# Kernel optimization log

Hardware: AMD Instinct MI355X
Metric: run time of the kernel (lower is better)

The kernel has to match this reference:

```python
import jax, jax.numpy as jnp
import numpy as np

SCALE = 10.0
TEMP = 0.5
SIM_TH = 0.7
EPOCH = 1
KL_WEIGHT = max(0.5 * (1 - EPOCH / 60), 0.1)
NEG_INF = -1e30


def _normalize(x, eps=1e-12):
    n = jnp.linalg.norm(x, axis=-1, keepdims=True)
    return x / jnp.maximum(n, eps)


def setup_inputs() -> dict:
    key = jax.random.key(0)
    ks = jax.random.split(key, 6)
    P, B, D, N, K = 4, 128, 512, 32768, 10
    # 0.02 scale keeps pairwise distances O(1) so exp(-SCALE*dist) does not underflow
    feature = jax.random.normal(ks[0], (P, B, D), jnp.float32) * 0.02
    text_feature = jax.random.normal(ks[1], (B, P, D), jnp.float32) * 0.02
    centers = jax.random.normal(ks[2], (P, N, D), jnp.float32) * 0.02
    position = jax.random.randint(ks[3], (B,), 0, N)
    cross_indices = jax.random.randint(ks[4], (B, K), 0, N)
    vid = jax.random.randint(ks[5], (N,), 0, 751)
    return {"feature": feature, "text_feature": text_feature, "centers": centers,
            "position": position, "cross_indices": cross_indices, "vid": vid}


def _align_loss(feature, text_feature):
    # feature: [P,B,D]; text_feature: [B,P,D] (detached in original)
    img = _normalize(feature)
    txt = _normalize(jax.lax.stop_gradient(jnp.transpose(text_feature, (1, 0, 2))))
    img_sim = jnp.einsum('pbd,pcd->pbc', img, img) / TEMP   # [P,B,B]
    txt_sim = jnp.einsum('pbd,pcd->pbc', txt, txt) / TEMP
    mask = (img_sim > SIM_TH) & (txt_sim > SIM_TH)
    valid = mask.any(-1)                                   # [P,B] row/col validity
    colm = valid[:, None, :]                               # mask over columns
    il = jnp.where(colm, img_sim, NEG_INF)
    tl = jnp.where(colm, txt_sim, NEG_INF)
    img_logp = jax.nn.log_softmax(il, -1)
    txt_logp = jax.nn.log_softmax(tl, -1)                  # fully detached (txt detached)
    txt_prob = jnp.exp(txt_logp)
    img_logp_sg = jax.lax.stop_gradient(img_logp)
    img_prob = jnp.exp(img_logp_sg)
    # F.kl_div(input=log q, target=p) = sum p*(log p - log q), batchmean over valid rows
    kl1 = jnp.sum(jnp.where(colm, txt_prob * (txt_logp - img_logp), 0.0), -1)      # [P,B]
    kl2 = jnp.sum(jnp.where(colm, img_prob * (img_logp_sg - txt_logp), 0.0), -1)
    nvalid = valid.sum(-1)                                 # [P]
    r1 = jnp.sum(jnp.where(valid, kl1, 0.0), -1)
    r2 = jnp.sum(jnp.where(valid, kl2, 0.0), -1)
    per_part = 0.5 * (r1 + r2) / jnp.maximum(nvalid, 1)
    return jnp.sum(jnp.where(nvalid > 0, per_part, 0.0))


def _contrastive_loss(feature, centers, position, cross_indices):
    P, B, D = feature.shape
    N = centers.shape[1]
    pos_feats = jnp.take(centers, cross_indices, axis=1)   # [P,B,K,D]
    fn2 = jnp.sum(feature * feature, -1)                   # [P,B]
    pn2 = jnp.sum(pos_feats * pos_feats, -1)               # [P,B,K]
    pd2 = fn2[..., None] + pn2 - 2.0 * jnp.einsum('pbd,pbkd->pbk', feature, pos_feats)
    pos_dist = jnp.sqrt(jnp.maximum(pd2, 1e-12))           # [P,B,K]
    cn2 = jnp.sum(centers * centers, -1)                   # [P,N]
    nd2 = fn2[..., None] + cn2[:, None, :] - 2.0 * jnp.einsum('pbd,pnd->pbn', feature, centers)
    neg_dist = jnp.sqrt(jnp.maximum(nd2, 1e-12))           # [P,B,N]
    neg_mask = (jnp.ones((N,), bool)
                .at[cross_indices.reshape(-1)].set(False)
                .at[position].set(False))
    x = jnp.log(jnp.sum(jnp.exp(-SCALE * pos_dist), -1))   # [P,B]
    ey = jnp.exp(-SCALE * neg_dist) * neg_mask[None, None, :].astype(neg_dist.dtype)
    y = jnp.log(jnp.sum(ey, -1))                           # [P,B]
    l = jnp.sum(y - x, -1) / B                             # per-part, div by feature.size(1)
    l = jnp.where(jnp.isnan(l), 0.0, l)
    return jnp.sum(l) / P


def reference(feature, text_feature, centers, position, cross_indices, vid):
    align_loss = _align_loss(feature, text_feature)
    contrastive_loss = _contrastive_loss(feature, centers, position, cross_indices)
    total_loss = contrastive_loss + KL_WEIGHT * align_loss
    pos_vid = jnp.take(vid, cross_indices, axis=0)         # [B,K]
    return total_loss, contrastive_loss, align_loss, pos_vid
```

## Files before the change

kernel.cpp:

```cpp
#include <hip/hip_runtime.h>
#include <hip/hip_bf16.h>
#include <math.h>

#define P_ 4
#define B_ 128
#define D_ 512
#define N_ 32768
#define K_ 10
#define TNB 128
#define NT2 (N_ / TNB)
#define BKC 64
#define KP 72

typedef __attribute__((ext_vector_type(8))) short bf16x8;
typedef __attribute__((ext_vector_type(4))) float f32x4;

static __device__ __forceinline__ float block_sum_128(float v, float* sh) {
    const int t = threadIdx.x;
    sh[t] = v; __syncthreads();
    #pragma unroll
    for (int s = 64; s > 0; s >>= 1) { if (t < s) sh[t] += sh[t + s]; __syncthreads(); }
    float r = sh[0]; __syncthreads();
    return r;
}

static __device__ __forceinline__ uint2 pack_bf16x4(float4 v) {
    union { __hip_bfloat162 h; unsigned u; } lo, hi;
    lo.h = __float22bfloat162_rn(make_float2(v.x, v.y));
    hi.h = __float22bfloat162_rn(make_float2(v.z, v.w));
    uint2 r; r.x = lo.u; r.y = hi.u;
    return r;
}

__global__ void prep_kernel(const float* __restrict__ feature,
                            unsigned short* __restrict__ featbf,
                            float* __restrict__ maskf) {
    int i = blockIdx.x * 256 + threadIdx.x;
    float4 v = ((const float4*)feature)[i];
    ((uint2*)featbf)[i] = pack_bf16x4(v);
    if (i < N_) maskf[i] = 1.0f;
}

__global__ void mask_zero_kernel(const int* __restrict__ cross,
                                 const int* __restrict__ pos,
                                 float* __restrict__ m) {
    int i = blockIdx.x * 256 + threadIdx.x;
    if (i < B_ * K_) m[cross[i]] = 0.0f;
    else if (i < B_ * K_ + B_) m[pos[i - B_ * K_]] = 0.0f;
}

__global__ void norm_kernel(const float* __restrict__ feature,
                            const float* __restrict__ text_feature,
                            float* __restrict__ img, float* __restrict__ txt,
                            float* __restrict__ fn2) {
    const int pb = blockIdx.x;
    const int p = pb >> 7, b = pb & 127;
    const int which = blockIdx.y;
    const int t = threadIdx.x;
    const float* src = (which == 0) ? feature + (size_t)pb * D_
                                    : text_feature + ((size_t)b * P_ + p) * D_;
    float v0 = src[t], v1 = src[t + 256];
    __shared__ float sred[256];
    sred[t] = v0 * v0 + v1 * v1;
    __syncthreads();
    #pragma unroll
    for (int s = 128; s > 0; s >>= 1) { if (t < s) sred[t] += sred[t + s]; __syncthreads(); }
    const float ss = sred[0];
    const float inv = 1.0f / fmaxf(sqrtf(ss), 1e-12f);
    float* dst = (which == 0) ? img : txt;
    dst[(size_t)pb * D_ + t] = v0 * inv;
    dst[(size_t)pb * D_ + t + 256] = v1 * inv;
    if (which == 0 && t == 0) fn2[pb] = ss;
}

__global__ void sim_kernel(const float* __restrict__ img,
                           const float* __restrict__ txt,
                           float* __restrict__ img_sim,
                           float* __restrict__ txt_sim,
                           float* __restrict__ validf) {
    const int p = blockIdx.x;
    const int b0 = blockIdx.y * 2;
    const int c = threadIdx.x;
    __shared__ float ai[2][D_];
    __shared__ float at[2][D_];
    __shared__ int flags[2];
    #pragma unroll
    for (int i = 0; i < 8; ++i) {
        int idx = c + i * 128;
        int row = idx >> 9, d = idx & 511;
        ai[row][d] = img[(size_t)(p * B_ + b0 + row) * D_ + d];
        at[row][d] = txt[(size_t)(p * B_ + b0 + row) * D_ + d];
    }
    if (c < 2) flags[c] = 0;
    __syncthreads();
    float di[2] = {0, 0};
    float dt[2] = {0, 0};
    const float* ic = img + (size_t)(p * B_ + c) * D_;
    const float* tc = txt + (size_t)(p * B_ + c) * D_;
    for (int d = 0; d < D_; d += 4) {
        float4 vi = *(const float4*)(ic + d);
        float4 vt = *(const float4*)(tc + d);
        #pragma unroll
        for (int i = 0; i < 2; ++i) {
            di[i] += ai[i][d] * vi.x + ai[i][d + 1] * vi.y + ai[i][d + 2] * vi.z + ai[i][d + 3] * vi.w;
            dt[i] += at[i][d] * vt.x + at[i][d + 1] * vt.y + at[i][d + 2] * vt.z + at[i][d + 3] * vt.w;
        }
    }
    #pragma unroll
    for (int i = 0; i < 2; ++i) {
        float is = 2.0f * di[i];
        float ts = 2.0f * dt[i];
        img_sim[(size_t)(p * B_ + b0 + i) * B_ + c] = is;
        txt_sim[(size_t)(p * B_ + b0 + i) * B_ + c] = ts;
        if (is > 0.7f && ts > 0.7f) flags[i] = 1;
    }
    __syncthreads();
    if (c < 2) validf[p * B_ + b0 + c] = (float)flags[c];
}

__global__ __launch_bounds__(256) void kl_kernel(
    const float* __restrict__ img_sim,
    const float* __restrict__ txt_sim,
    const float* __restrict__ validf,
    float* __restrict__ klrow) {
    const int l = threadIdx.x & 63;
    const int wv = threadIdx.x >> 6;
    const int p = blockIdx.x;
    const int r = blockIdx.y * 4 + wv;
    const size_t base = (size_t)(p * B_ + r) * B_;
    const bool v0 = validf[p * B_ + l] > 0.5f;
    const bool v1 = validf[p * B_ + 64 + l] > 0.5f;
    const float il0 = v0 ? img_sim[base + l] : -1e30f;
    const float il1 = v1 ? img_sim[base + 64 + l] : -1e30f;
    const float tl0 = v0 ? txt_sim[base + l] : -1e30f;
    const float tl1 = v1 ? txt_sim[base + 64 + l] : -1e30f;
    float mi = fmaxf(il0, il1), mt = fmaxf(tl0, tl1);
    #pragma unroll
    for (int off = 32; off > 0; off >>= 1) {
        mi = fmaxf(mi, __shfl_xor(mi, off));
        mt = fmaxf(mt, __shfl_xor(mt, off));
    }
    float si = expf(il0 - mi) + expf(il1 - mi);
    float st = expf(tl0 - mt) + expf(tl1 - mt);
    #pragma unroll
    for (int off = 32; off > 0; off >>= 1) {
        si += __shfl_xor(si, off);
        st += __shfl_xor(st, off);
    }
    const float lsei = mi + logf(si);
    const float lset = mt + logf(st);
    float term = 0.0f;
    if (v0) {
        float lpi = il0 - lsei, lpt = tl0 - lset;
        term += expf(lpt) * (lpt - lpi) + expf(lpi) * (lpi - lpt);
    }
    if (v1) {
        float lpi = il1 - lsei, lpt = tl1 - lset;
        term += expf(lpt) * (lpt - lpi) + expf(lpi) * (lpi - lpt);
    }
    #pragma unroll
    for (int off = 32; off > 0; off >>= 1) term += __shfl_xor(term, off);
    if (l == 0) klrow[p * B_ + r] = (validf[p * B_ + r] > 0.5f) ? term : 0.0f;
}

__global__ void posx_kernel(const float* __restrict__ feature,
                            const float* __restrict__ centers,
                            const float* __restrict__ fn2,
                            const int* __restrict__ cross,
                            float* __restrict__ xarr) {
    const int pb = blockIdx.x;
    const int p = pb >> 7, b = pb & 127;
    const int l = threadIdx.x;
    const float* f = feature + (size_t)pb * D_;
    float4 f0 = *(const float4*)(f + l * 4);
    float4 f1 = *(const float4*)(f + 256 + l * 4);
    const float fn2v = fn2[pb];
    float ex = 0.0f;
    #pragma unroll
    for (int k = 0; k < K_; ++k) {
        int idx = cross[b * K_ + k];
        const float* cp = centers + ((size_t)p * N_ + idx) * D_;
        float4 c0 = *(const float4*)(cp + l * 4);
        float4 c1 = *(const float4*)(cp + 256 + l * 4);
        float dot = f0.x * c0.x + f0.y * c0.y + f0.z * c0.z + f0.w * c0.w
                  + f1.x * c1.x + f1.y * c1.y + f1.z * c1.z + f1.w * c1.w;
        float pn2 = c0.x * c0.x + c0.y * c0.y + c0.z * c0.z + c0.w * c0.w
                  + c1.x * c1.x + c1.y * c1.y + c1.z * c1.z + c1.w * c1.w;
        #pragma unroll
        for (int off = 32; off > 0; off >>= 1) {
            dot += __shfl_down(dot, off);
            pn2 += __shfl_down(pn2, off);
        }
        if (l == 0) {
            float d2 = fn2v + pn2 - 2.0f * dot;
            ex += expf(-10.0f * sqrtf(fmaxf(d2, 1e-12f)));
        }
    }
    if (l == 0) xarr[pb] = logf(ex);
}

__global__ __launch_bounds__(256) void neg_mfma_kernel(
    const unsigned short* __restrict__ featbf,
    const float* __restrict__ centers,
    const float* __restrict__ fn2,
    const float* __restrict__ maskf,
    float* __restrict__ Spart) {
    const int tile = blockIdx.x;
    const int p = blockIdx.y;
    const int n0g = tile * TNB;
    const int t = threadIdx.x;
    const int l = t & 63;
    const int w = t >> 6;
    const int m0w = (w & 1) * 64;
    const int n0w = (w >> 1) * 64;

    __shared__ unsigned short Bs[2][128 * KP];
    __shared__ float cn2s[128];
    __shared__ float red[128];
    __shared__ float fn2s[128];

    if (t < 128) { red[t] = 0.0f; fn2s[t] = fn2[p * B_ + t]; }

    f32x4 acc[4][4];
    #pragma unroll
    for (int i = 0; i < 4; ++i)
        #pragma unroll
        for (int j = 0; j < 4; ++j) acc[i][j] = (f32x4)0.0f;

    float c2acc[8];
    #pragma unroll
    for (int i = 0; i < 8; ++i) c2acc[i] = 0.0f;

    const unsigned short* Ab = featbf + (size_t)p * B_ * D_;
    const float* Bb = centers + ((size_t)p * N_ + n0g) * D_;

    const int lrow = t >> 4;
    const int c4 = t & 15;

    float4 vb[8];
    #pragma unroll
    for (int i = 0; i < 8; ++i)
        vb[i] = *(const float4*)(Bb + (size_t)(lrow + i * 16) * D_ + c4 * 4);
    #pragma unroll
    for (int i = 0; i < 8; ++i) {
        const int row = lrow + i * 16;
        *(uint2*)&Bs[0][row * KP + c4 * 4] = pack_bf16x4(vb[i]);
        c2acc[i] += vb[i].x * vb[i].x + vb[i].y * vb[i].y
                  + vb[i].z * vb[i].z + vb[i].w * vb[i].w;
    }
    __syncthreads();

    for (int kk = 0; kk < D_; kk += BKC) {
        const int cur = (kk >> 6) & 1;
        const int nxt = cur ^ 1;
        const bool more = (kk + BKC) < D_;
        if (more) {
            #pragma unroll
            for (int i = 0; i < 8; ++i)
                vb[i] = *(const float4*)(Bb + (size_t)(lrow + i * 16) * D_ + (kk + BKC) + c4 * 4);
        }
        #pragma unroll
        for (int ks = 0; ks < 2; ++ks) {
            bf16x8 af[4], bfr[4];
            const int ko = ks * 32 + (l >> 4) * 8;
            #pragma unroll
            for (int i = 0; i < 4; ++i) {
                af[i]  = *(const bf16x8*)(Ab + (size_t)(m0w + i * 16 + (l & 15)) * D_ + kk + ko);
                bfr[i] = *(const bf16x8*)&Bs[cur][(n0w + i * 16 + (l & 15)) * KP + ko];
            }
            #pragma unroll
            for (int i = 0; i < 4; ++i)
                #pragma unroll
                for (int j = 0; j < 4; ++j)
                    acc[i][j] = __builtin_amdgcn_mfma_f32_16x16x32_bf16(
                        af[i], bfr[j], acc[i][j], 0, 0, 0);
        }
        if (more) {
            #pragma unroll
            for (int i = 0; i < 8; ++i) {
                const int row = lrow + i * 16;
                *(uint2*)&Bs[nxt][row * KP + c4 * 4] = pack_bf16x4(vb[i]);
                c2acc[i] += vb[i].x * vb[i].x + vb[i].y * vb[i].y
                          + vb[i].z * vb[i].z + vb[i].w * vb[i].w;
            }
        }
        __syncthreads();
    }

    #pragma unroll
    for (int i = 0; i < 8; ++i) {
        float s = c2acc[i];
        s += __shfl_xor(s, 1); s += __shfl_xor(s, 2);
        s += __shfl_xor(s, 4); s += __shfl_xor(s, 8);
        if (c4 == 0) cn2s[lrow + i * 16] = s;
    }
    __syncthreads();

    float c2l[4], mkl[4];
    #pragma unroll
    for (int j = 0; j < 4; ++j) {
        const int col = n0w + j * 16 + (l & 15);
        c2l[j] = cn2s[col];
        mkl[j] = maskf[n0g + col];
    }
    #pragma unroll
    for (int i = 0; i < 4; ++i) {
        #pragma unroll
        for (int r = 0; r < 4; ++r) {
            const int row = m0w + i * 16 + (l >> 4) * 4 + r;
            const float fv = fn2s[row];
            float s = 0.0f;
            #pragma unroll
            for (int j = 0; j < 4; ++j) {
                const float nd2 = fv + c2l[j] - 2.0f * acc[i][j][r];
                s += mkl[j] * __expf(-10.0f * sqrtf(fmaxf(nd2, 1e-12f)));
            }
            s += __shfl_xor(s, 1); s += __shfl_xor(s, 2);
            s += __shfl_xor(s, 4); s += __shfl_xor(s, 8);
            if ((l & 15) == 0) atomicAdd(&red[row], s);
        }
    }
    __syncthreads();
    if (t < 128) Spart[(size_t)(p * B_ + t) * NT2 + tile] = red[t];
}

__global__ void red_kernel(const float* __restrict__ Spart,
                           const float* __restrict__ xarr,
                           float* __restrict__ diff) {
    const int pb = blockIdx.x;
    const int t = threadIdx.x;
    __shared__ float sh[128];
    const float* sp = Spart + (size_t)pb * NT2;
    float s = sp[t] + sp[t + 128];
    float S = block_sum_128(s, sh);
    if (t == 0) diff[pb] = logf(S) - xarr[pb];
}

__global__ void final_kernel(const float* __restrict__ validf,
                             const float* __restrict__ klrow,
                             const float* __restrict__ diff,
                             float* __restrict__ out) {
    const int t = threadIdx.x;
    __shared__ float sh[128];
    __shared__ float accum[2];
    if (t == 0) { accum[0] = 0.0f; accum[1] = 0.0f; }
    __syncthreads();
    for (int p = 0; p < P_; ++p) {
        float nv = block_sum_128(validf[p * B_ + t], sh);
        float ks = block_sum_128(klrow[p * B_ + t], sh);
        float ds = block_sum_128(diff[p * B_ + t], sh);
        if (t == 0) {
            float lp = ds / (float)B_;
            if (!(lp != lp)) accum[0] += lp;
            if (nv > 0.5f) accum[1] += 0.5f * ks / fmaxf(nv, 1.0f);
        }
        __syncthreads();
    }
    if (t == 0) {
        float contrastive = accum[0] / (float)P_;
        float align = accum[1];
        out[1] = contrastive;
        out[2] = align;
        out[0] = contrastive + 0.49166666666666664f * align;
    }
}

__global__ void posvid_kernel(const int* __restrict__ cross,
                              const int* __restrict__ vid,
                              float* __restrict__ out) {
    int i = blockIdx.x * 256 + threadIdx.x;
    if (i < B_ * K_) out[3 + i] = (float)vid[cross[i]];
}

extern "C" void kernel_launch(void* const* d_in, const int* in_sizes, int n_in,
                              void* d_out, int out_size, void* d_ws, size_t ws_size,
                              hipStream_t stream) {
    const float* feature      = (const float*)d_in[0];
    const float* text_feature = (const float*)d_in[1];
    const float* centers      = (const float*)d_in[2];
    const int*   position     = (const int*)d_in[3];
    const int*   cross        = (const int*)d_in[4];
    const int*   vid          = (const int*)d_in[5];
    float* out = (float*)d_out;

    float* ws      = (float*)d_ws;
    float* img     = ws;
    float* txt     = img + (size_t)P_ * B_ * D_;
    float* fn2     = txt + (size_t)P_ * B_ * D_;
    float* img_sim = fn2 + P_ * B_;
    float* txt_sim = img_sim + P_ * B_ * B_;
    float* validf  = txt_sim + P_ * B_ * B_;
    float* klrow   = validf + P_ * B_;
    float* xarr    = klrow + P_ * B_;
    float* maskf   = xarr + P_ * B_;
    float* diff    = maskf + N_;
    float* Spart   = diff + P_ * B_;
    unsigned short* featbf = (unsigned short*)(Spart + (size_t)P_ * B_ * NT2);

    prep_kernel<<<P_ * B_ * D_ / 4 / 256, 256, 0, stream>>>(feature, featbf, maskf);
    mask_zero_kernel<<<(B_ * K_ + B_ + 255) / 256, 256, 0, stream>>>(cross, position, maskf);
    norm_kernel<<<dim3(P_ * B_, 2), 256, 0, stream>>>(feature, text_feature, img, txt, fn2);
    sim_kernel<<<dim3(P_, B_ / 2), 128, 0, stream>>>(img, txt, img_sim, txt_sim, validf);
    kl_kernel<<<dim3(P_, B_ / 4), 256, 0, stream>>>(img_sim, txt_sim, validf, klrow);
    posx_kernel<<<P_ * B_, 64, 0, stream>>>(feature, centers, fn2, cross, xarr);
    neg_mfma_kernel<<<dim3(NT2, P_), 256, 0, stream>>>(featbf, centers, fn2, maskf, Spart);
    red_kernel<<<P_ * B_, 128, 0, stream>>>(Spart, xarr, diff);
    final_kernel<<<1, 128, 0, stream>>>(validf, klrow, diff, out);
    posvid_kernel<<<(B_ * K_ + 255) / 256, 256, 0, stream>>>(cross, vid, out);
}
```

Baseline: 457.6 us.

## Stage feature tiles in LDS inside MFMA kernel and merge small kernels

```diff
diff --git a/kernel.cpp b/kernel.cpp
--- a/kernel.cpp
+++ b/kernel.cpp
@@ -9,8 +9,9 @@
 #define K_ 10
 #define TNB 128
 #define NT2 (N_ / TNB)
-#define BKC 64
-#define KP 72
+#define BK2 32
+#define NCH (D_ / BK2)
+#define KP2 40
 
 typedef __attribute__((ext_vector_type(8))) short bf16x8;
 typedef __attribute__((ext_vector_type(4))) float f32x4;
@@ -32,15 +33,10 @@
     return r;
 }
 
-__global__ void prep_kernel(const float* __restrict__ feature,
-                            unsigned short* __restrict__ featbf,
-                            float* __restrict__ maskf) {
+__global__ void mask_init_kernel(float* __restrict__ m) {
     int i = blockIdx.x * 256 + threadIdx.x;
-    float4 v = ((const float4*)feature)[i];
-    ((uint2*)featbf)[i] = pack_bf16x4(v);
-    if (i < N_) maskf[i] = 1.0f;
-}
-
+    if (i < N_) m[i] = 1.0f;
+}
 __global__ void mask_zero_kernel(const int* __restrict__ cross,
                                  const int* __restrict__ pos,
                                  float* __restrict__ m) {
@@ -200,7 +196,7 @@
 }
 
 __global__ __launch_bounds__(256) void neg_mfma_kernel(
-    const unsigned short* __restrict__ featbf,
+    const float* __restrict__ feature,
     const float* __restrict__ centers,
     const float* __restrict__ fn2,
     const float* __restrict__ maskf,
@@ -214,7 +210,8 @@
     const int m0w = (w & 1) * 64;
     const int n0w = (w >> 1) * 64;
 
-    __shared__ unsigned short Bs[2][128 * KP];
+    __shared__ unsigned short As[2][128 * KP2];
+    __shared__ unsigned short Bs[2][128 * KP2];
     __shared__ float cn2s[128];
     __shared__ float red[128];
     __shared__ float fn2s[128];
@@ -227,59 +224,61 @@
         #pragma unroll
         for (int j = 0; j < 4; ++j) acc[i][j] = (f32x4)0.0f;
 
-    float c2acc[8];
-    #pragma unroll
-    for (int i = 0; i < 8; ++i) c2acc[i] = 0.0f;
-
-    const unsigned short* Ab = featbf + (size_t)p * B_ * D_;
+    float c2acc[4] = {0.0f, 0.0f, 0.0f, 0.0f};
+
+    const float* Ab = feature + (size_t)p * B_ * D_;
     const float* Bb = centers + ((size_t)p * N_ + n0g) * D_;
 
-    const int lrow = t >> 4;
-    const int c4 = t & 15;
-
-    float4 vb[8];
-    #pragma unroll
-    for (int i = 0; i < 8; ++i)
-        vb[i] = *(const float4*)(Bb + (size_t)(lrow + i * 16) * D_ + c4 * 4);
-    #pragma unroll
-    for (int i = 0; i < 8; ++i) {
-        const int row = lrow + i * 16;
-        *(uint2*)&Bs[0][row * KP + c4 * 4] = pack_bf16x4(vb[i]);
+    const int f8 = t & 7;
+    const int r0 = t >> 3;
+
+    float4 va[4], vb[4];
+    #pragma unroll
+    for (int i = 0; i < 4; ++i) {
+        const int row = r0 + 32 * i;
+        va[i] = *(const float4*)(Ab + (size_t)row * D_ + f8 * 4);
+        vb[i] = *(const float4*)(Bb + (size_t)row * D_ + f8 * 4);
+    }
+    #pragma unroll
+    for (int i = 0; i < 4; ++i) {
+        const int row = r0 + 32 * i;
+        *(uint2*)&As[0][row * KP2 + f8 * 4] = pack_bf16x4(va[i]);
+        *(uint2*)&Bs[0][row * KP2 + f8 * 4] = pack_bf16x4(vb[i]);
         c2acc[i] += vb[i].x * vb[i].x + vb[i].y * vb[i].y
                   + vb[i].z * vb[i].z + vb[i].w * vb[i].w;
     }
     __syncthreads();
 
-    for (int kk = 0; kk < D_; kk += BKC) {
-        const int cur = (kk >> 6) & 1;
-        const int nxt = cur ^ 1;
-        const bool more = (kk + BKC) < D_;
-        if (more) {
-            #pragma unroll
-            for (int i = 0; i < 8; ++i)
-                vb[i] = *(const float4*)(Bb + (size_t)(lrow + i * 16) * D_ + (kk + BKC) + c4 * 4);
-        }
-        #pragma unroll
-        for (int ks = 0; ks < 2; ++ks) {
-            bf16x8 af[4], bfr[4];
-            const int ko = ks * 32 + (l >> 4) * 8;
+    const int ko = (l >> 4) * 8;
+    for (int c = 0; c < NCH; ++c) {
+        const int cur = c & 1, nxt = cur ^ 1;
+        const int kk = (c + 1) * BK2;
+        if (c < NCH - 1) {
             #pragma unroll
             for (int i = 0; i < 4; ++i) {
-                af[i]  = *(const bf16x8*)(Ab + (size_t)(m0w + i * 16 + (l & 15)) * D_ + kk + ko);
-                bfr[i] = *(const bf16x8*)&Bs[cur][(n0w + i * 16 + (l & 15)) * KP + ko];
+                const int row = r0 + 32 * i;
+                va[i] = *(const float4*)(Ab + (size_t)row * D_ + kk + f8 * 4);
+                vb[i] = *(const float4*)(Bb + (size_t)row * D_ + kk + f8 * 4);
             }
+        }
+        bf16x8 af[4], bfr[4];
+        #pragma unroll
+        for (int i = 0; i < 4; ++i) {
+            af[i]  = *(const bf16x8*)&As[cur][(m0w + i * 16 + (l & 15)) * KP2 + ko];
+            bfr[i] = *(const bf16x8*)&Bs[cur][(n0w + i * 16 + (l & 15)) * KP2 + ko];
+        }
+        #pragma unroll
+        for (int i = 0; i < 4; ++i)
             #pragma unroll
-            for (int i = 0; i < 4; ++i)
-                #pragma unroll
-                for (int j = 0; j < 4; ++j)
-                    acc[i][j] = __builtin_amdgcn_mfma_f32_16x16x32_bf16(
-                        af[i], bfr[j], acc[i][j], 0, 0, 0);
-        }
-        if (more) {
+            for (int j = 0; j < 4; ++j)
+                acc[i][j] = __builtin_amdgcn_mfma_f32_16x16x32_bf16(
+                    af[i], bfr[j], acc[i][j], 0, 0, 0);
+        if (c < NCH - 1) {
             #pragma unroll
-            for (int i = 0; i < 8; ++i) {
-                const int row = lrow + i * 16;
-                *(uint2*)&Bs[nxt][row * KP + c4 * 4] = pack_bf16x4(vb[i]);
+            for (int i = 0; i < 4; ++i) {
+                const int row = r0 + 32 * i;
+                *(uint2*)&As[nxt][row * KP2 + f8 * 4] = pack_bf16x4(va[i]);
+                *(uint2*)&Bs[nxt][row * KP2 + f8 * 4] = pack_bf16x4(vb[i]);
                 c2acc[i] += vb[i].x * vb[i].x + vb[i].y * vb[i].y
                           + vb[i].z * vb[i].z + vb[i].w * vb[i].w;
             }
@@ -288,11 +287,10 @@
     }
 
     #pragma unroll
-    for (int i = 0; i < 8; ++i) {
+    for (int i = 0; i < 4; ++i) {
         float s = c2acc[i];
-        s += __shfl_xor(s, 1); s += __shfl_xor(s, 2);
-        s += __shfl_xor(s, 4); s += __shfl_xor(s, 8);
-        if (c4 == 0) cn2s[lrow + i * 16] = s;
+        s += __shfl_xor(s, 1); s += __shfl_xor(s, 2); s += __shfl_xor(s, 4);
+        if (f8 == 0) cn2s[r0 + 32 * i] = s;
     }
     __syncthreads();
 
@@ -339,6 +337,8 @@
 __global__ void final_kernel(const float* __restrict__ validf,
                              const float* __restrict__ klrow,
                              const float* __restrict__ diff,
+                             const int* __restrict__ cross,
+                             const int* __restrict__ vid,
                              float* __restrict__ out) {
     const int t = threadIdx.x;
     __shared__ float sh[128];
@@ -363,13 +363,11 @@
         out[2] = align;
         out[0] = contrastive + 0.49166666666666664f * align;
     }
-}
-
-__global__ void posvid_kernel(const int* __restrict__ cross,
-                              const int* __restrict__ vid,
-                              float* __restrict__ out) {
-    int i = blockIdx.x * 256 + threadIdx.x;
-    if (i < B_ * K_) out[3 + i] = (float)vid[cross[i]];
+    #pragma unroll
+    for (int k = 0; k < K_; ++k) {
+        const int i = k * 128 + t;
+        out[3 + i] = (float)vid[cross[i]];
+    }
 }
 
 extern "C" void kernel_launch(void* const* d_in, const int* in_sizes, int n_in,
@@ -395,16 +393,14 @@
     float* maskf   = xarr + P_ * B_;
     float* diff    = maskf + N_;
     float* Spart   = diff + P_ * B_;
-    unsigned short* featbf = (unsigned short*)(Spart + (size_t)P_ * B_ * NT2);
-
-    prep_kernel<<<P_ * B_ * D_ / 4 / 256, 256, 0, stream>>>(feature, featbf, maskf);
+
+    mask_init_kernel<<<N_ / 256, 256, 0, stream>>>(maskf);
     mask_zero_kernel<<<(B_ * K_ + B_ + 255) / 256, 256, 0, stream>>>(cross, position, maskf);
     norm_kernel<<<dim3(P_ * B_, 2), 256, 0, stream>>>(feature, text_feature, img, txt, fn2);
     sim_kernel<<<dim3(P_, B_ / 2), 128, 0, stream>>>(img, txt, img_sim, txt_sim, validf);
     kl_kernel<<<dim3(P_, B_ / 4), 256, 0, stream>>>(img_sim, txt_sim, validf, klrow);
     posx_kernel<<<P_ * B_, 64, 0, stream>>>(feature, centers, fn2, cross, xarr);
-    neg_mfma_kernel<<<dim3(NT2, P_), 256, 0, stream>>>(featbf, centers, fn2, maskf, Spart);
+    neg_mfma_kernel<<<dim3(NT2, P_), 256, 0, stream>>>(feature, centers, fn2, maskf, Spart);
     red_kernel<<<P_ * B_, 128, 0, stream>>>(Spart, xarr, diff);
-    final_kernel<<<1, 128, 0, stream>>>(validf, klrow, diff, out);
-    posvid_kernel<<<(B_ * K_ + 255) / 256, 256, 0, stream>>>(cross, vid, out);
-}
+    final_kernel<<<1, 128, 0, stream>>>(validf, klrow, diff, cross, vid, out);
+}
```

After: 446.6 us. -2.4%, faster.
